# Optimization experiments

Hardware: AMD Instinct MI355X
Metric: run time of the kernel (lower is better)

## Reference

```python
import jax, jax.numpy as jnp
import numpy as np

N = 8192
IN_F = 512
OUT_F = 256


def setup_inputs() -> dict:
    key = jax.random.key(0)
    k1, k2, k3, k4 = jax.random.split(key, 4)
    return {
        "input": jax.random.normal(k1, (N, IN_F), dtype=jnp.float32),
        "w_s": jax.random.uniform(k2, (N, 1), dtype=jnp.float32),
        "w_r": jax.random.uniform(k3, (N, 1), dtype=jnp.float32),
        "weight": jax.random.normal(k4, (IN_F, OUT_F), dtype=jnp.float32),
    }


def reference(input, w_s, w_r, weight):
    # rank-1 learned adjacency: G = w_s @ w_r^T, symmetrized with abs
    G = w_s @ w_r.T                                  # [N, N]
    aG = jnp.abs(G)
    A = (aG + aG.T) * 0.5                            # symmetric_graph
    # normalise_graph: zero the diagonal (graph - diag(graph)*eye)
    idx = jnp.arange(A.shape[0])
    A = A.at[idx, idx].set(0.0)
    # symmetric degree normalization D^-1/2 A D^-1/2 as row/col scaling
    s = A.sum(axis=1)
    s = jnp.where(s == 0.0, 1.0, s)
    dinv = s ** -0.5                                 # [N]
    normA = dinv[:, None] * A * dinv[None, :]        # == D @ A @ D
    # GCN propagation
    H = input @ weight                               # [N, OUT_F]
    return normA @ H
```

## Files before the change

### kernel.cpp

```cpp
#include <hip/hip_runtime.h>
#include <hip/hip_bf16.h>

#define NR 8192
#define KF 512
#define OF 256

#define WS_AL   0
#define WS_BE   8192
#define WS_GA   16384
#define WS_PU   24576
#define WS_PV   90112
#define WS_U    155648
#define WS_V    155904
#define HB_BYTE_OFF 624640

typedef float f32x4 __attribute__((ext_vector_type(4)));
typedef __bf16 bf16x8 __attribute__((ext_vector_type(8)));

__global__ __launch_bounds__(512, 1) void k1(const float* __restrict__ input,
                                             const float* __restrict__ w_s,
                                             const float* __restrict__ w_r,
                                             const float* __restrict__ weight,
                                             float* __restrict__ ws,
                                             __hip_bfloat16* __restrict__ HbH) {
    __shared__ float H[32 * 257];
    __shared__ __bf16 Wt[256][136];
    __shared__ float pl[32], ql[32];
    __shared__ float red[16];

    const int tid  = threadIdx.x;
    const int blk  = blockIdx.x;
    const int base = blk * 32;
    __bf16* Hb = (__bf16*)HbH;

    float la = 0.f, lb = 0.f;
#pragma unroll
    for (int i = 0; i < 16; ++i) {
        const int idx = tid + (i << 9);
        la += fabsf(w_s[idx]);
        lb += fabsf(w_r[idx]);
    }
#pragma unroll
    for (int o = 32; o > 0; o >>= 1) {
        la += __shfl_down(la, o);
        lb += __shfl_down(lb, o);
    }
    if ((tid & 63) == 0) { red[tid >> 6] = la; red[8 + (tid >> 6)] = lb; }
    __syncthreads();
    float Sa = 0.f, Sb = 0.f;
#pragma unroll
    for (int i = 0; i < 8; ++i) { Sa += red[i]; Sb += red[8 + i]; }

    if (tid < 32) {
        const int row = base + tid;
        const float a = fabsf(w_s[row]);
        const float b = fabsf(w_r[row]);
        float s = 0.5f * (a * (Sb - b) + b * (Sa - a));
        if (s == 0.f) s = 1.f;
        const float d = 1.0f / sqrtf(s);
        ws[WS_AL + row] = 0.5f * d * a;
        ws[WS_BE + row] = 0.5f * d * b;
        ws[WS_GA + row] = d * d * a * b;
        pl[tid] = d * b;
        ql[tid] = d * a;
    }
    __syncthreads();

    const int w       = tid >> 6;
    const int l       = tid & 63;
    const int rowhalf = w >> 2;
    const int cgrp    = w & 3;
    const int lrow    = l & 15;
    const int khalf   = l >> 4;

    f32x4 acc0 = {0.f,0.f,0.f,0.f}, acc1 = {0.f,0.f,0.f,0.f};
    f32x4 acc2 = {0.f,0.f,0.f,0.f}, acc3 = {0.f,0.f,0.f,0.f};

    const int cW  = tid & 255;
    const int kg0 = tid >> 8;

    for (int ch = 0; ch < 4; ++ch) {
#pragma unroll
        for (int j = 0; j < 8; ++j) {
            const int k0 = (kg0 + 2 * j) * 8;
            const int kg = ch * 128 + k0;
            bf16x8 v;
#pragma unroll
            for (int jj = 0; jj < 8; ++jj)
                v[jj] = (__bf16)weight[(kg + jj) * OF + cW];
            *(bf16x8*)&Wt[cW][k0] = v;
        }
        __syncthreads();
#pragma unroll
        for (int kst = 0; kst < 4; ++kst) {
            const int klocal = kst * 32 + khalf * 8;
            const int kglob  = ch * 128 + klocal;
            const float* ap = input + (base + rowhalf * 16 + lrow) * KF + kglob;
            const f32x4 alo = *(const f32x4*)ap;
            const f32x4 ahi = *(const f32x4*)(ap + 4);
            bf16x8 af;
            af[0]=(__bf16)alo[0]; af[1]=(__bf16)alo[1]; af[2]=(__bf16)alo[2]; af[3]=(__bf16)alo[3];
            af[4]=(__bf16)ahi[0]; af[5]=(__bf16)ahi[1]; af[6]=(__bf16)ahi[2]; af[7]=(__bf16)ahi[3];
            const bf16x8 b0 = *(const bf16x8*)&Wt[cgrp * 64 +  0 + lrow][klocal];
            const bf16x8 b1 = *(const bf16x8*)&Wt[cgrp * 64 + 16 + lrow][klocal];
            const bf16x8 b2 = *(const bf16x8*)&Wt[cgrp * 64 + 32 + lrow][klocal];
            const bf16x8 b3 = *(const bf16x8*)&Wt[cgrp * 64 + 48 + lrow][klocal];
            acc0 = __builtin_amdgcn_mfma_f32_16x16x32_bf16(af, b0, acc0, 0, 0, 0);
            acc1 = __builtin_amdgcn_mfma_f32_16x16x32_bf16(af, b1, acc1, 0, 0, 0);
            acc2 = __builtin_amdgcn_mfma_f32_16x16x32_bf16(af, b2, acc2, 0, 0, 0);
            acc3 = __builtin_amdgcn_mfma_f32_16x16x32_bf16(af, b3, acc3, 0, 0, 0);
        }
        __syncthreads();
    }

    {
        const int hr = rowhalf * 16 + khalf * 4;
        const int hc = cgrp * 64 + lrow;
#pragma unroll
        for (int r = 0; r < 4; ++r) {
            H[(hr + r) * 257 + hc +  0] = acc0[r];
            H[(hr + r) * 257 + hc + 16] = acc1[r];
            H[(hr + r) * 257 + hc + 32] = acc2[r];
            H[(hr + r) * 257 + hc + 48] = acc3[r];
        }
    }
    __syncthreads();

    {
        const int k = tid & 255;
        const float* pv = (tid < 256) ? pl : ql;
        float u = 0.f;
#pragma unroll 8
        for (int r = 0; r < 32; ++r) u += pv[r] * H[r * 257 + k];
        if (tid < 256) ws[WS_PU + blk * 256 + k] = u;
        else           ws[WS_PV + blk * 256 + k] = u;
    }

    {
        const int row = tid & 31;
        const int c0  = (tid >> 5) * 16;
        const float* hp = &H[row * 257 + c0];
        bf16x8 v0, v1;
#pragma unroll
        for (int j = 0; j < 8; ++j) v0[j] = (__bf16)hp[j];
#pragma unroll
        for (int j = 0; j < 8; ++j) v1[j] = (__bf16)hp[8 + j];
        __bf16* dst = Hb + (base + row) * OF + c0;
        *(bf16x8*)dst       = v0;
        *(bf16x8*)(dst + 8) = v1;
    }
}

__global__ __launch_bounds__(256) void k2(float* __restrict__ ws) {
    const int b   = blockIdx.x;
    const bool isV = b >= 8;
    const int kb  = (b & 7) * 32;
    const int t   = threadIdx.x;
    const int k   = kb + (t >> 3);
    const int p0  = t & 7;
    const float* P = ws + (isV ? WS_PV : WS_PU);
    float s = 0.f;
#pragma unroll 8
    for (int j = p0; j < 256; j += 8) s += P[j * 256 + k];
#pragma unroll
    for (int o = 4; o > 0; o >>= 1) s += __shfl_down(s, o, 8);
    if (p0 == 0) ws[(isV ? WS_V : WS_U) + k] = s;
}

__global__ __launch_bounds__(256) void k3(const __hip_bfloat16* __restrict__ HbH,
                                          const float* __restrict__ ws,
                                          float* __restrict__ out) {
    __shared__ float aL[32], bL[32], gL[32], UL[256], VL[256];
    const int tid  = threadIdx.x;
    const int base = blockIdx.x * 32;
    UL[tid] = ws[WS_U + tid];
    VL[tid] = ws[WS_V + tid];
    if (tid < 32) {
        aL[tid] = ws[WS_AL + base + tid];
        bL[tid] = ws[WS_BE + base + tid];
        gL[tid] = ws[WS_GA + base + tid];
    }
    __syncthreads();
    const ushort* Hb = (const ushort*)HbH;
    const int kp = (tid & 127) * 2;
    const int rh = tid >> 7;
    const float u0 = UL[kp], u1 = UL[kp + 1];
    const float v0 = VL[kp], v1 = VL[kp + 1];
#pragma unroll
    for (int i = 0; i < 16; ++i) {
        const int r = rh * 16 + i;
        const unsigned u = *(const unsigned*)(Hb + (base + r) * OF + kp);
        const float h0 = __uint_as_float(u << 16);
        const float h1 = __uint_as_float(u & 0xffff0000u);
        float2 o;
        o.x = aL[r] * u0 + bL[r] * v0 - gL[r] * h0;
        o.y = aL[r] * u1 + bL[r] * v1 - gL[r] * h1;
        *(float2*)(out + (base + r) * OF + kp) = o;
    }
}

extern "C" void kernel_launch(void* const* d_in, const int* in_sizes, int n_in,
                              void* d_out, int out_size, void* d_ws, size_t ws_size,
                              hipStream_t stream) {
    const float* input  = (const float*)d_in[0];
    const float* w_s    = (const float*)d_in[1];
    const float* w_r    = (const float*)d_in[2];
    const float* weight = (const float*)d_in[3];
    float* ws = (float*)d_ws;
    __hip_bfloat16* Hb = (__hip_bfloat16*)((char*)d_ws + HB_BYTE_OFF);
    float* out = (float*)d_out;

    hipLaunchKernelGGL(k1, dim3(256), dim3(512), 0, stream, input, w_s, w_r, weight, ws, Hb);
    hipLaunchKernelGGL(k2, dim3(16),  dim3(256), 0, stream, ws);
    hipLaunchKernelGGL(k3, dim3(256), dim3(256), 0, stream, Hb, ws, out);
}
```

Baseline: 92.64 us.

## Pre-transpose weight to bf16 once and stream B operand from global

Adds a small kernel that converts and transposes the weight matrix into bf16 [OUT][IN] layout once. Previously each of the 256 GEMM blocks re-read and converted the full weight matrix into shared memory with strided scalar loads. The GEMM kernel now reads the B fragments directly from global/L2 with vector loads, which removes the shared-memory staging and its syncs. It also vectorizes the w_s/w_r abs-sum loads and widens the output kernel's stores to float4. The cost is one extra kernel launch, and the B reads now depend on L2 hit rate.

```diff
diff --git a/kernel.cpp b/kernel.cpp
--- a/kernel.cpp
+++ b/kernel.cpp
@@ -13,18 +13,47 @@
 #define WS_U    155648
 #define WS_V    155904
 #define HB_BYTE_OFF 624640
+#define BT_BYTE_OFF (HB_BYTE_OFF + 4194304)
 
 typedef float f32x4 __attribute__((ext_vector_type(4)));
 typedef __bf16 bf16x8 __attribute__((ext_vector_type(8)));
 
-__global__ __launch_bounds__(512, 1) void k1(const float* __restrict__ input,
-                                             const float* __restrict__ w_s,
-                                             const float* __restrict__ w_r,
-                                             const float* __restrict__ weight,
-                                             float* __restrict__ ws,
-                                             __hip_bfloat16* __restrict__ HbH) {
+__global__ __launch_bounds__(256) void kW(const float* __restrict__ weight,
+                                          __hip_bfloat16* __restrict__ BtH) {
+    __shared__ float tile[64][65];
+    const int t   = blockIdx.x;
+    const int k0  = (t & 7) * 64;
+    const int c0  = (t >> 3) * 64;
+    const int tid = threadIdx.x;
+    const int cc  = (tid & 15) * 4;
+    const int kr0 = tid >> 4;
+#pragma unroll
+    for (int it = 0; it < 4; ++it) {
+        const int kr = it * 16 + kr0;
+        const f32x4 v = *(const f32x4*)(weight + (k0 + kr) * OF + c0 + cc);
+        tile[kr][cc + 0] = v[0]; tile[kr][cc + 1] = v[1];
+        tile[kr][cc + 2] = v[2]; tile[kr][cc + 3] = v[3];
+    }
+    __syncthreads();
+    __bf16* Bt = (__bf16*)BtH;
+    const int cr = tid >> 2;
+    const int kq = (tid & 3) * 16;
+#pragma unroll
+    for (int h = 0; h < 2; ++h) {
+        bf16x8 v;
+#pragma unroll
+        for (int j = 0; j < 8; ++j) v[j] = (__bf16)tile[kq + h * 8 + j][cr];
+        *(bf16x8*)(Bt + (c0 + cr) * KF + k0 + kq + h * 8) = v;
+    }
+}
+
+__global__ __launch_bounds__(512) void k1(const float* __restrict__ input,
+                                          const float* __restrict__ w_s,
+                                          const float* __restrict__ w_r,
+                                          const __hip_bfloat16* __restrict__ BtH,
+                                          float* __restrict__ ws,
+                                          __hip_bfloat16* __restrict__ HbH) {
     __shared__ float H[32 * 257];
-    __shared__ __bf16 Wt[256][136];
     __shared__ float pl[32], ql[32];
     __shared__ float red[16];
 
@@ -32,13 +61,18 @@
     const int blk  = blockIdx.x;
     const int base = blk * 32;
     __bf16* Hb = (__bf16*)HbH;
+    const __bf16* Bt = (const __bf16*)BtH;
 
     float la = 0.f, lb = 0.f;
-#pragma unroll
-    for (int i = 0; i < 16; ++i) {
-        const int idx = tid + (i << 9);
-        la += fabsf(w_s[idx]);
-        lb += fabsf(w_r[idx]);
+    {
+        const int t4 = tid * 4;
+#pragma unroll
+        for (int i = 0; i < 4; ++i) {
+            const f32x4 va = *(const f32x4*)(w_s + i * 2048 + t4);
+            const f32x4 vb = *(const f32x4*)(w_r + i * 2048 + t4);
+            la += fabsf(va[0]) + fabsf(va[1]) + fabsf(va[2]) + fabsf(va[3]);
+            lb += fabsf(vb[0]) + fabsf(vb[1]) + fabsf(vb[2]) + fabsf(vb[3]);
+        }
     }
 #pragma unroll
     for (int o = 32; o > 0; o >>= 1) {
@@ -64,7 +98,6 @@
         pl[tid] = d * b;
         ql[tid] = d * a;
     }
-    __syncthreads();
 
     const int w       = tid >> 6;
     const int l       = tid & 63;
@@ -73,44 +106,27 @@
     const int lrow    = l & 15;
     const int khalf   = l >> 4;
 
+    const float*  ap0 = input + (base + rowhalf * 16 + lrow) * KF + khalf * 8;
+    const __bf16* bp0 = Bt + (cgrp * 64 + lrow) * KF + khalf * 8;
+
     f32x4 acc0 = {0.f,0.f,0.f,0.f}, acc1 = {0.f,0.f,0.f,0.f};
     f32x4 acc2 = {0.f,0.f,0.f,0.f}, acc3 = {0.f,0.f,0.f,0.f};
-
-    const int cW  = tid & 255;
-    const int kg0 = tid >> 8;
-
-    for (int ch = 0; ch < 4; ++ch) {
-#pragma unroll
-        for (int j = 0; j < 8; ++j) {
-            const int k0 = (kg0 + 2 * j) * 8;
-            const int kg = ch * 128 + k0;
-            bf16x8 v;
-#pragma unroll
-            for (int jj = 0; jj < 8; ++jj)
-                v[jj] = (__bf16)weight[(kg + jj) * OF + cW];
-            *(bf16x8*)&Wt[cW][k0] = v;
-        }
-        __syncthreads();
-#pragma unroll
-        for (int kst = 0; kst < 4; ++kst) {
-            const int klocal = kst * 32 + khalf * 8;
-            const int kglob  = ch * 128 + klocal;
-            const float* ap = input + (base + rowhalf * 16 + lrow) * KF + kglob;
-            const f32x4 alo = *(const f32x4*)ap;
-            const f32x4 ahi = *(const f32x4*)(ap + 4);
-            bf16x8 af;
-            af[0]=(__bf16)alo[0]; af[1]=(__bf16)alo[1]; af[2]=(__bf16)alo[2]; af[3]=(__bf16)alo[3];
-            af[4]=(__bf16)ahi[0]; af[5]=(__bf16)ahi[1]; af[6]=(__bf16)ahi[2]; af[7]=(__bf16)ahi[3];
-            const bf16x8 b0 = *(const bf16x8*)&Wt[cgrp * 64 +  0 + lrow][klocal];
-            const bf16x8 b1 = *(const bf16x8*)&Wt[cgrp * 64 + 16 + lrow][klocal];
-            const bf16x8 b2 = *(const bf16x8*)&Wt[cgrp * 64 + 32 + lrow][klocal];
-            const bf16x8 b3 = *(const bf16x8*)&Wt[cgrp * 64 + 48 + lrow][klocal];
-            acc0 = __builtin_amdgcn_mfma_f32_16x16x32_bf16(af, b0, acc0, 0, 0, 0);
-            acc1 = __builtin_amdgcn_mfma_f32_16x16x32_bf16(af, b1, acc1, 0, 0, 0);
-            acc2 = __builtin_amdgcn_mfma_f32_16x16x32_bf16(af, b2, acc2, 0, 0, 0);
-            acc3 = __builtin_amdgcn_mfma_f32_16x16x32_bf16(af, b3, acc3, 0, 0, 0);
-        }
-        __syncthreads();
+#pragma unroll
+    for (int ks = 0; ks < 16; ++ks) {
+        const int k0 = ks * 32;
+        const f32x4 alo = *(const f32x4*)(ap0 + k0);
+        const f32x4 ahi = *(const f32x4*)(ap0 + k0 + 4);
+        bf16x8 af;
+        af[0]=(__bf16)alo[0]; af[1]=(__bf16)alo[1]; af[2]=(__bf16)alo[2]; af[3]=(__bf16)alo[3];
+        af[4]=(__bf16)ahi[0]; af[5]=(__bf16)ahi[1]; af[6]=(__bf16)ahi[2]; af[7]=(__bf16)ahi[3];
+        const bf16x8 b0 = *(const bf16x8*)(bp0 + 0 * 16 * KF + k0);
+        const bf16x8 b1 = *(const bf16x8*)(bp0 + 1 * 16 * KF + k0);
+        const bf16x8 b2 = *(const bf16x8*)(bp0 + 2 * 16 * KF + k0);
+        const bf16x8 b3 = *(const bf16x8*)(bp0 + 3 * 16 * KF + k0);
+        acc0 = __builtin_amdgcn_mfma_f32_16x16x32_bf16(af, b0, acc0, 0, 0, 0);
+        acc1 = __builtin_amdgcn_mfma_f32_16x16x32_bf16(af, b1, acc1, 0, 0, 0);
+        acc2 = __builtin_amdgcn_mfma_f32_16x16x32_bf16(af, b2, acc2, 0, 0, 0);
+        acc3 = __builtin_amdgcn_mfma_f32_16x16x32_bf16(af, b3, acc3, 0, 0, 0);
     }
 
     {
@@ -152,12 +168,12 @@
 }
 
 __global__ __launch_bounds__(256) void k2(float* __restrict__ ws) {
-    const int b   = blockIdx.x;
+    const int b    = blockIdx.x;
     const bool isV = b >= 8;
-    const int kb  = (b & 7) * 32;
-    const int t   = threadIdx.x;
-    const int k   = kb + (t >> 3);
-    const int p0  = t & 7;
+    const int kb   = (b & 7) * 32;
+    const int t    = threadIdx.x;
+    const int k    = kb + (t >> 3);
+    const int p0   = t & 7;
     const float* P = ws + (isV ? WS_PV : WS_PU);
     float s = 0.f;
 #pragma unroll 8
@@ -182,20 +198,25 @@
     }
     __syncthreads();
     const ushort* Hb = (const ushort*)HbH;
-    const int kp = (tid & 127) * 2;
-    const int rh = tid >> 7;
-    const float u0 = UL[kp], u1 = UL[kp + 1];
-    const float v0 = VL[kp], v1 = VL[kp + 1];
-#pragma unroll
-    for (int i = 0; i < 16; ++i) {
-        const int r = rh * 16 + i;
-        const unsigned u = *(const unsigned*)(Hb + (base + r) * OF + kp);
-        const float h0 = __uint_as_float(u << 16);
-        const float h1 = __uint_as_float(u & 0xffff0000u);
-        float2 o;
-        o.x = aL[r] * u0 + bL[r] * v0 - gL[r] * h0;
-        o.y = aL[r] * u1 + bL[r] * v1 - gL[r] * h1;
-        *(float2*)(out + (base + r) * OF + kp) = o;
+    const int c4 = (tid & 63) * 4;
+    const int r0 = (tid >> 6) * 8;
+    const float u0 = UL[c4], u1 = UL[c4+1], u2 = UL[c4+2], u3 = UL[c4+3];
+    const float v0 = VL[c4], v1 = VL[c4+1], v2 = VL[c4+2], v3 = VL[c4+3];
+#pragma unroll
+    for (int i = 0; i < 8; ++i) {
+        const int r = r0 + i;
+        const uint2 hv = *(const uint2*)(Hb + (base + r) * OF + c4);
+        const float h0 = __uint_as_float(hv.x << 16);
+        const float h1 = __uint_as_float(hv.x & 0xffff0000u);
+        const float h2 = __uint_as_float(hv.y << 16);
+        const float h3 = __uint_as_float(hv.y & 0xffff0000u);
+        const float A = aL[r], B = bL[r], G = gL[r];
+        f32x4 o;
+        o[0] = A * u0 + B * v0 - G * h0;
+        o[1] = A * u1 + B * v1 - G * h1;
+        o[2] = A * u2 + B * v2 - G * h2;
+        o[3] = A * u3 + B * v3 - G * h3;
+        *(f32x4*)(out + (base + r) * OF + c4) = o;
     }
 }
 
@@ -208,9 +229,11 @@
     const float* weight = (const float*)d_in[3];
     float* ws = (float*)d_ws;
     __hip_bfloat16* Hb = (__hip_bfloat16*)((char*)d_ws + HB_BYTE_OFF);
+    __hip_bfloat16* Bt = (__hip_bfloat16*)((char*)d_ws + BT_BYTE_OFF);
     float* out = (float*)d_out;
 
-    hipLaunchKernelGGL(k1, dim3(256), dim3(512), 0, stream, input, w_s, w_r, weight, ws, Hb);
+    hipLaunchKernelGGL(kW, dim3(32),  dim3(256), 0, stream, weight, Bt);
+    hipLaunchKernelGGL(k1, dim3(256), dim3(512), 0, stream, input, w_s, w_r, Bt, ws, Hb);
     hipLaunchKernelGGL(k2, dim3(16),  dim3(256), 0, stream, ws);
     hipLaunchKernelGGL(k3, dim3(256), dim3(256), 0, stream, Hb, ws, out);
 }
```

Measured after the change: 99.60 us. 1.08x slower.
